# Performance work log

Hardware: AMD Instinct MI355X
Metric: run time of the kernel (lower is better)

Reference implementation:

```python
import jax, jax.numpy as jnp
import numpy as np

N_ITEMS = 100000
N_USERS = 40000
EMB = 100
NNZ_A = 3200000
NNZ_U = 1600000
BATCH = 4096
LAYERS = 3


def setup_inputs() -> dict:
    key = jax.random.key(0)
    ks = jax.random.split(key, 9)
    return {
        "adj_vals": jax.random.uniform(ks[0], (NNZ_A,), dtype=jnp.float32),
        "u_vals": jax.random.uniform(ks[1], (NNZ_U,), dtype=jnp.float32),
        "embedding": jax.random.normal(ks[2], (N_ITEMS, EMB), dtype=jnp.float32),
        "user_embedding": jax.random.normal(ks[3], (N_USERS, EMB), dtype=jnp.float32),
        "adj_rows": jax.random.randint(ks[4], (NNZ_A,), 0, N_ITEMS),
        "adj_cols": jax.random.randint(ks[5], (NNZ_A,), 0, N_ITEMS),
        "u_rows": jax.random.randint(ks[6], (NNZ_U,), 0, N_USERS),
        "u_cols": jax.random.randint(ks[7], (NNZ_U,), 0, N_ITEMS),
        "user": jax.random.randint(ks[8], (BATCH,), 0, N_USERS),
    }


def spmm(vals, rows, cols, x, n_rows):
    # COO sparse (n_rows x n_cols) @ dense x: gather rows of x by col index,
    # scale by nnz values, scatter-add into output rows.
    return jax.ops.segment_sum(vals[:, None] * x[cols], rows, num_segments=n_rows)


def reference(adj_vals, u_vals, embedding, user_embedding,
              adj_rows, adj_cols, u_rows, u_cols, user):
    # Multi-hop hypergraph propagation with running layer-sum (final = sum of layers 0..L)
    x = embedding
    total = x
    for _ in range(LAYERS):
        x = spmm(adj_vals, adj_rows, adj_cols, x, embedding.shape[0])
        total = total + x
    # ishyper branch: user embeddings = (u_adj @ summed item embeddings)[user]
    user_all = spmm(u_vals, u_rows, u_cols, total, user_embedding.shape[0])
    return total, user_all[user]
```

## Files before the change

### kernel.cpp

```cpp
#include <hip/hip_runtime.h>
#include <stdint.h>

#define EMB 100
#define HW 50
#define V4_PER_ROW 25
#define BSHIFT 8
#define NBMAX 1024
#define TP 256
#define EP 16

static __device__ __forceinline__ uint32_t pack_bf16(float a, float b) {
    uint32_t ua = __float_as_uint(a);
    uint32_t ub = __float_as_uint(b);
    ua = (ua + 0x7FFFu + ((ua >> 16) & 1u)) >> 16;
    ub = (ub + 0x7FFFu + ((ub >> 16) & 1u)) >> 16;
    return ua | (ub << 16);
}
static __device__ __forceinline__ float bflo(uint32_t p) { return __uint_as_float(p << 16); }
static __device__ __forceinline__ float bfhi(uint32_t p) { return __uint_as_float(p & 0xFFFF0000u); }

__global__ void convert_bf16(const float2* __restrict__ x, uint32_t* __restrict__ xbf, int nwords) {
    for (int i = blockIdx.x * blockDim.x + threadIdx.x; i < nwords; i += gridDim.x * blockDim.x) {
        float2 v = x[i];
        xbf[i] = pack_bf16(v.x, v.y);
    }
}

__global__ void map_build(const int* __restrict__ user, uint32_t* __restrict__ map, int batch) {
    int i = blockIdx.x * blockDim.x + threadIdx.x;
    if (i < batch) atomicMin(&map[user[i]], (uint32_t)i);
}

__global__ __launch_bounds__(TP) void pass1_count(
    const int* __restrict__ ra, int na, const int* __restrict__ ru, int nu,
    const uint32_t* __restrict__ map, int* __restrict__ countsT,
    int nblk, int nbA, int nbTot)
{
    __shared__ int lc[NBMAX];
    const int blk = blockIdx.x;
    for (int i = threadIdx.x; i < nbTot; i += TP) lc[i] = 0;
    __syncthreads();
    const int base = blk * (TP * EP);
    const int n = na + nu;
    for (int i = 0; i < EP; ++i) {
        int e = base + i * TP + threadIdx.x;
        int b = -1;
        if (e < na) {
            b = __builtin_nontemporal_load(ra + e) >> BSHIFT;
        } else if (e < n) {
            int r = __builtin_nontemporal_load(ru + (e - na));
            if (map[r] != 0xFFFFFFFFu) b = nbA + (r >> BSHIFT);
        }
        if (b >= 0) atomicAdd(&lc[b], 1);
    }
    __syncthreads();
    for (int i = threadIdx.x; i < nbTot; i += TP)
        countsT[(size_t)i * nblk + blk] = lc[i];
}

#define SCAN_T 256
#define SCAN_E 16

__global__ void scan_blocks(const int* __restrict__ in, int* __restrict__ out,
                            int* __restrict__ sums, int n) {
    __shared__ int smem[SCAN_T];
    const int b = blockIdx.x, tid = threadIdx.x;
    const int base = b * SCAN_T * SCAN_E + tid * SCAN_E;
    int loc[SCAN_E];
    int s = 0;
    for (int i = 0; i < SCAN_E; ++i) {
        int idx = base + i;
        int v = (idx < n) ? in[idx] : 0;
        loc[i] = s; s += v;
    }
    smem[tid] = s; __syncthreads();
    for (int off = 1; off < SCAN_T; off <<= 1) {
        int v = (tid >= off) ? smem[tid - off] : 0;
        __syncthreads();
        smem[tid] += v;
        __syncthreads();
    }
    int pre = (tid == 0) ? 0 : smem[tid - 1];
    if (tid == SCAN_T - 1) sums[b] = smem[tid];
    for (int i = 0; i < SCAN_E; ++i) {
        int idx = base + i;
        if (idx < n) out[idx] = pre + loc[i];
    }
}

__global__ void scan_mid(int* __restrict__ sums, int nb, int* __restrict__ total_out) {
    __shared__ int sh[256];
    const int t = threadIdx.x;
    int v = (t < nb) ? sums[t] : 0;
    sh[t] = v; __syncthreads();
    for (int off = 1; off < 256; off <<= 1) {
        int u = (t >= off) ? sh[t - off] : 0;
        __syncthreads();
        sh[t] += u;
        __syncthreads();
    }
    if (t < nb) sums[t] = sh[t];
    if (t == 255) *total_out = sh[255];
}

__global__ void scan_fixup(int* __restrict__ out, const int* __restrict__ sums, int n) {
    const int b = blockIdx.x;
    if (b == 0) return;
    const int add = sums[b - 1];
    const int base = b * SCAN_T * SCAN_E + threadIdx.x * SCAN_E;
    for (int i = 0; i < SCAN_E; ++i) {
        int idx = base + i;
        if (idx < n) out[idx] += add;
    }
}

__global__ void extract_bases(const int* __restrict__ scanned, int nblk, int nbTot,
                              const int* __restrict__ total, int* __restrict__ bases,
                              int* __restrict__ rpA_end, int nnzA, int* __restrict__ rpU_end) {
    int t = blockIdx.x * blockDim.x + threadIdx.x;
    if (t < nbTot) bases[t] = scanned[(size_t)t * nblk];
    if (t == 0) {
        int tot = *total;
        bases[nbTot] = tot;
        *rpA_end = nnzA;
        *rpU_end = tot - nnzA;
    }
}

__global__ __launch_bounds__(TP) void pass2_scatter(
    const float* __restrict__ va, const int* __restrict__ ra, const int* __restrict__ ia, int na,
    const float* __restrict__ vu, const int* __restrict__ ru, const int* __restrict__ iu, int nu,
    const uint32_t* __restrict__ map, const int* __restrict__ scanned,
    uint2* __restrict__ tmp, int nblk, int nbA, int nbTot)
{
    __shared__ int cur[NBMAX];
    const int blk = blockIdx.x;
    for (int i = threadIdx.x; i < nbTot; i += TP)
        cur[i] = scanned[(size_t)i * nblk + blk];
    __syncthreads();
    const int base = blk * (TP * EP);
    const int n = na + nu;
    for (int i = 0; i < EP; ++i) {
        int e = base + i * TP + threadIdx.x;
        if (e < na) {
            int r = __builtin_nontemporal_load(ra + e);
            int p = atomicAdd(&cur[r >> BSHIFT], 1);
            uint32_t key = ((uint32_t)(r & 255) << 17) | (uint32_t)__builtin_nontemporal_load(ia + e);
            tmp[p] = make_uint2(key, (uint32_t)__float_as_uint(__builtin_nontemporal_load(va + e)));
        } else if (e < n) {
            int k = e - na;
            int r = __builtin_nontemporal_load(ru + k);
            if (map[r] == 0xFFFFFFFFu) continue;
            int p = atomicAdd(&cur[nbA + (r >> BSHIFT)], 1);
            uint32_t key = ((uint32_t)(r & 255) << 17) | (uint32_t)__builtin_nontemporal_load(iu + k);
            tmp[p] = make_uint2(key, (uint32_t)__float_as_uint(__builtin_nontemporal_load(vu + k)));
        }
    }
}

__global__ __launch_bounds__(1024) void bucket_sort(const uint2* __restrict__ tmp,
                                                    const int* __restrict__ bases,
                                                    uint32_t* __restrict__ pk,
                                                    int* __restrict__ rpA, int* __restrict__ rpU,
                                                    int nbA, int nnzA, int nItems, int nUsers) {
    __shared__ int h[256];
    __shared__ int cur[256];
    const int t = threadIdx.x;
    const int b = blockIdx.x;
    const int lo = bases[b], hi = bases[b + 1];
    const bool isU = (b >= nbA);
    const int rowbase = (isU ? (b - nbA) : b) << BSHIFT;

    if (t < 256) h[t] = 0;
    __syncthreads();
    for (int i = lo + t; i < hi; i += 1024)
        atomicAdd(&h[tmp[i].x >> 17], 1);
    __syncthreads();
    int cnt = (t < 256) ? h[t] : 0;
    for (int off = 1; off < 256; off <<= 1) {
        int u = (t < 256 && t >= off) ? h[t - off] : 0;
        __syncthreads();
        if (t < 256) h[t] += u;
        __syncthreads();
    }
    if (t < 256) {
        int gpos = lo + h[t] - cnt;
        int row = rowbase + t;
        if (isU) { if (row < nUsers) rpU[row] = gpos - nnzA; }
        else     { if (row < nItems) rpA[row] = gpos; }
        cur[t] = gpos;
    }
    __syncthreads();
    for (int i = lo + t; i < hi; i += 1024) {
        uint2 e = tmp[i];
        int rl = (int)(e.x >> 17);
        uint32_t col = e.x & 0x1FFFFu;
        int p = atomicAdd(&cur[rl], 1);
        float v = __uint_as_float(e.y);
        uint32_t q = (uint32_t)(v * 32767.0f + 0.5f);
        if (q > 32767u) q = 32767u;
        pk[p] = (col << 15) | q;
    }
}

#define DECODE(w, v, c) { v = (float)((w) & 0x7FFFu) * (1.0f/32767.0f); c = (int)((w) >> 15); }

__global__ __launch_bounds__(256) void spmm_pk(
    const uint32_t* __restrict__ pk, const int* __restrict__ rowptr,
    const uint32_t* __restrict__ xbf, uint32_t* __restrict__ outbf,
    const float2* __restrict__ emb2, const uint32_t* __restrict__ x1bf,
    const uint32_t* __restrict__ x2bf, float2* __restrict__ total2,
    uint32_t* __restrict__ totbf, int nrows)
{
    const int wid = (blockIdx.x * blockDim.x + threadIdx.x) >> 6;
    const int lane = threadIdx.x & 63;
    if (wid >= nrows) return;
    const int start = rowptr[wid], end = rowptr[wid + 1];
    float a0 = 0.f, a1 = 0.f;
    for (int base = start; base < end; base += 64) {
        const int nc = min(64, end - base);
        uint32_t w = 0;
        if (lane < nc) w = __builtin_nontemporal_load(pk + base + lane);
        float myv; int myc;
        DECODE(w, myv, myc);
        int t = 0;
        for (; t + 4 <= nc; t += 4) {
            float v0 = __shfl(myv, t),     v1 = __shfl(myv, t + 1);
            float v2 = __shfl(myv, t + 2), v3 = __shfl(myv, t + 3);
            int   c0 = __shfl(myc, t),     c1 = __shfl(myc, t + 1);
            int   c2 = __shfl(myc, t + 2), c3 = __shfl(myc, t + 3);
            uint32_t p0 = 0, p1 = 0, p2 = 0, p3 = 0;
            if (lane < HW) {
                p0 = xbf[(size_t)c0 * HW + lane];
                p1 = xbf[(size_t)c1 * HW + lane];
                p2 = xbf[(size_t)c2 * HW + lane];
                p3 = xbf[(size_t)c3 * HW + lane];
            }
            a0 = fmaf(v0, bflo(p0), a0); a1 = fmaf(v0, bfhi(p0), a1);
            a0 = fmaf(v1, bflo(p1), a0); a1 = fmaf(v1, bfhi(p1), a1);
            a0 = fmaf(v2, bflo(p2), a0); a1 = fmaf(v2, bfhi(p2), a1);
            a0 = fmaf(v3, bflo(p3), a0); a1 = fmaf(v3, bfhi(p3), a1);
        }
        for (; t < nc; ++t) {
            float v0 = __shfl(myv, t);
            int c0 = __shfl(myc, t);
            uint32_t p0 = 0;
            if (lane < HW) p0 = xbf[(size_t)c0 * HW + lane];
            a0 = fmaf(v0, bflo(p0), a0);
            a1 = fmaf(v0, bfhi(p0), a1);
        }
    }
    if (lane < HW) {
        const size_t widx = (size_t)wid * HW + lane;
        if (outbf) outbf[widx] = pack_bf16(a0, a1);
        if (total2) {
            float2 e = emb2[widx];
            uint32_t w1 = x1bf[widx], w2 = x2bf[widx];
            float t0 = e.x + bflo(w1) + bflo(w2) + a0;
            float t1 = e.y + bfhi(w1) + bfhi(w2) + a1;
            total2[widx] = make_float2(t0, t1);
            totbf[widx] = pack_bf16(t0, t1);
        }
    }
}

__global__ __launch_bounds__(256) void spmm_batch_pk(
    const uint32_t* __restrict__ pk, const int* __restrict__ rowptr,
    const int* __restrict__ user, const uint32_t* __restrict__ xbf,
    float2* __restrict__ out2, int batch)
{
    const int wid = (blockIdx.x * blockDim.x + threadIdx.x) >> 6;
    const int lane = threadIdx.x & 63;
    if (wid >= batch) return;
    const int row = user[wid];
    const int start = rowptr[row], end = rowptr[row + 1];
    float a0 = 0.f, a1 = 0.f;
    for (int base = start; base < end; base += 64) {
        const int nc = min(64, end - base);
        uint32_t w = 0;
        if (lane < nc) w = __builtin_nontemporal_load(pk + base + lane);
        float myv; int myc;
        DECODE(w, myv, myc);
        int t = 0;
        for (; t + 4 <= nc; t += 4) {
            float v0 = __shfl(myv, t),     v1 = __shfl(myv, t + 1);
            float v2 = __shfl(myv, t + 2), v3 = __shfl(myv, t + 3);
            int   c0 = __shfl(myc, t),     c1 = __shfl(myc, t + 1);
            int   c2 = __shfl(myc, t + 2), c3 = __shfl(myc, t + 3);
            uint32_t p0 = 0, p1 = 0, p2 = 0, p3 = 0;
            if (lane < HW) {
                p0 = xbf[(size_t)c0 * HW + lane];
                p1 = xbf[(size_t)c1 * HW + lane];
                p2 = xbf[(size_t)c2 * HW + lane];
                p3 = xbf[(size_t)c3 * HW + lane];
            }
            a0 = fmaf(v0, bflo(p0), a0); a1 = fmaf(v0, bfhi(p0), a1);
            a0 = fmaf(v1, bflo(p1), a0); a1 = fmaf(v1, bfhi(p1), a1);
            a0 = fmaf(v2, bflo(p2), a0); a1 = fmaf(v2, bfhi(p2), a1);
            a0 = fmaf(v3, bflo(p3), a0); a1 = fmaf(v3, bfhi(p3), a1);
        }
        for (; t < nc; ++t) {
            float v0 = __shfl(myv, t);
            int c0 = __shfl(myc, t);
            uint32_t p0 = 0;
            if (lane < HW) p0 = xbf[(size_t)c0 * HW + lane];
            a0 = fmaf(v0, bflo(p0), a0);
            a1 = fmaf(v0, bfhi(p0), a1);
        }
    }
    if (lane < HW) out2[(size_t)wid * HW + lane] = make_float2(a0, a1);
}

__global__ void spmm_scatter(const float* __restrict__ vals, const int* __restrict__ rows,
                             const int* __restrict__ cols, const float* __restrict__ x,
                             float* __restrict__ out, int nnz) {
    long long t = (long long)blockIdx.x * blockDim.x + threadIdx.x;
    int e = (int)(t / V4_PER_ROW);
    int c = (int)(t % V4_PER_ROW);
    if (e >= nnz) return;
    int col = cols[e]; int row = rows[e]; float v = vals[e];
    const float4 g = *(const float4*)(x + (size_t)col * EMB + c * 4);
    float* o = out + (size_t)row * EMB + c * 4;
    atomicAdd(o + 0, v * g.x); atomicAdd(o + 1, v * g.y);
    atomicAdd(o + 2, v * g.z); atomicAdd(o + 3, v * g.w);
}
__global__ void add_inplace(float* __restrict__ acc, const float* __restrict__ x, int n4) {
    int i = blockIdx.x * blockDim.x + threadIdx.x;
    if (i < n4) {
        float4 a = ((const float4*)acc)[i];
        const float4 b = ((const float4*)x)[i];
        a.x += b.x; a.y += b.y; a.z += b.z; a.w += b.w;
        ((float4*)acc)[i] = a;
    }
}
__global__ void gather_rows(const float* __restrict__ src, const int* __restrict__ idx,
                            float* __restrict__ out, int nrows) {
    int t = blockIdx.x * blockDim.x + threadIdx.x;
    int r = t / V4_PER_ROW, c = t % V4_PER_ROW;
    if (r >= nrows) return;
    int s = idx[r];
    *(float4*)(out + (size_t)r * EMB + c * 4) = *(const float4*)(src + (size_t)s * EMB + c * 4);
}

static inline size_t align256(size_t x) { return (x + 255) & ~(size_t)255; }

extern "C" void kernel_launch(void* const* d_in, const int* in_sizes, int n_in,
                              void* d_out, int out_size, void* d_ws, size_t ws_size,
                              hipStream_t stream) {
    const float* adj_vals  = (const float*)d_in[0];
    const float* u_vals    = (const float*)d_in[1];
    const float* embedding = (const float*)d_in[2];
    const int*   adj_rows  = (const int*)d_in[4];
    const int*   adj_cols  = (const int*)d_in[5];
    const int*   u_rows    = (const int*)d_in[6];
    const int*   u_cols    = (const int*)d_in[7];
    const int*   user      = (const int*)d_in[8];

    const int NNZ_A   = in_sizes[0];
    const int NNZ_U   = in_sizes[1];
    const int N_ITEMS = in_sizes[2] / EMB;
    const int N_USERS = in_sizes[3] / EMB;
    const int BATCH   = in_sizes[8];

    const int NB_A = (N_ITEMS + 255) >> BSHIFT;
    const int NB_U = (N_USERS + 255) >> BSHIFT;
    const int NB_TOT = NB_A + NB_U;

    const int NNZ_T = NNZ_A + NNZ_U;
    const int nblk = (NNZ_T + TP * EP - 1) / (TP * EP);
    const long long nScan = (long long)NB_TOT * nblk;
    const int nsb = (int)((nScan + SCAN_T * SCAN_E - 1) / (SCAN_T * SCAN_E));

    float* total    = (float*)d_out;
    float* out_user = total + (size_t)N_ITEMS * EMB;

    const size_t rowWords = (size_t)N_ITEMS * HW;

    size_t off = 0;
    char* ws = (char*)d_ws;
    #define WS_ALLOC(name, bytes) char* name = ws + off; off += align256(bytes)
    WS_ALLOC(p_r0,      2 * rowWords * 4);
    WS_ALLOC(p_ebf,     rowWords * 4);
    WS_ALLOC(p_pk,      (size_t)NNZ_T * 4);
    WS_ALLOC(p_rpA,     ((size_t)N_ITEMS + 1) * 4);
    WS_ALLOC(p_rpU,     ((size_t)N_USERS + 1) * 4);
    WS_ALLOC(p_map,     (size_t)N_USERS * 4);
    WS_ALLOC(p_countsT, (size_t)nScan * 4);
    WS_ALLOC(p_sums,    256 * 4);
    WS_ALLOC(p_total,   4);
    WS_ALLOC(p_bases,   ((size_t)NB_TOT + 1) * 4);
    #undef WS_ALLOC
    const size_t tmpBytes = (size_t)NNZ_T * 8;

    if (ws_size >= off && tmpBytes <= 2 * rowWords * 4 && NB_TOT <= NBMAX && nsb <= 256) {
        uint32_t* x1bf  = (uint32_t*)p_r0;
        uint32_t* x2bf  = (uint32_t*)(p_r0 + rowWords * 4);
        uint2*    tmp   = (uint2*)p_r0;
        uint32_t* embbf = (uint32_t*)p_ebf;
        uint32_t* totbf = (uint32_t*)p_ebf;
        uint32_t* pk    = (uint32_t*)p_pk;
        int* rpA = (int*)p_rpA;
        int* rpU = (int*)p_rpU;
        uint32_t* map = (uint32_t*)p_map;
        int* countsT = (int*)p_countsT;
        int* sums    = (int*)p_sums;
        int* totalN  = (int*)p_total;
        int* bases   = (int*)p_bases;

        hipMemsetAsync(map, 0xFF, (size_t)N_USERS * 4, stream);
        map_build<<<(BATCH + 255) / 256, 256, 0, stream>>>(user, map, BATCH);

        convert_bf16<<<2048, 256, 0, stream>>>((const float2*)embedding, embbf, (int)rowWords);

        pass1_count<<<nblk, TP, 0, stream>>>(adj_rows, NNZ_A, u_rows, NNZ_U, map,
                                             countsT, nblk, NB_A, NB_TOT);
        scan_blocks<<<nsb, SCAN_T, 0, stream>>>(countsT, countsT, sums, (int)nScan);
        scan_mid<<<1, 256, 0, stream>>>(sums, nsb, totalN);
        scan_fixup<<<nsb, SCAN_T, 0, stream>>>(countsT, sums, (int)nScan);
        extract_bases<<<(NB_TOT + 255) / 256, 256, 0, stream>>>(countsT, nblk, NB_TOT, totalN,
                                                                bases, rpA + N_ITEMS, NNZ_A,
                                                                rpU + N_USERS);
        pass2_scatter<<<nblk, TP, 0, stream>>>(adj_vals, adj_rows, adj_cols, NNZ_A,
                                               u_vals, u_rows, u_cols, NNZ_U,
                                               map, countsT, tmp, nblk, NB_A, NB_TOT);
        bucket_sort<<<NB_TOT, 1024, 0, stream>>>(tmp, bases, pk, rpA, rpU,
                                                 NB_A, NNZ_A, N_ITEMS, N_USERS);

        const int gridA = (N_ITEMS + 3) / 4;
        spmm_pk<<<gridA, 256, 0, stream>>>(pk, rpA, embbf, x1bf,
                                           nullptr, nullptr, nullptr, nullptr, nullptr, N_ITEMS);
        spmm_pk<<<gridA, 256, 0, stream>>>(pk, rpA, x1bf, x2bf,
                                           nullptr, nullptr, nullptr, nullptr, nullptr, N_ITEMS);
        spmm_pk<<<gridA, 256, 0, stream>>>(pk, rpA, x2bf, nullptr,
                                           (const float2*)embedding, x1bf, x2bf,
                                           (float2*)total, totbf, N_ITEMS);
        const int gridB = (BATCH + 3) / 4;
        spmm_batch_pk<<<gridB, 256, 0, stream>>>(pk + NNZ_A, rpU, user, totbf,
                                                 (float2*)out_user, BATCH);
    } else {
        const size_t itemBytes = (size_t)N_ITEMS * EMB * sizeof(float);
        float* buf0 = (float*)d_ws;
        float* buf1 = buf0 + (size_t)N_ITEMS * EMB;
        float* user_all = buf1;
        const size_t userBytes = (size_t)N_USERS * EMB * sizeof(float);

        hipMemcpyAsync(total, embedding, itemBytes, hipMemcpyDeviceToDevice, stream);
        const int blkA = (NNZ_A * V4_PER_ROW + 255) / 256;
        const int blkU = (NNZ_U * V4_PER_ROW + 255) / 256;
        const int n4 = N_ITEMS * EMB / 4;
        const int blkAdd = (n4 + 255) / 256;

        hipMemsetAsync(buf0, 0, itemBytes, stream);
        spmm_scatter<<<blkA, 256, 0, stream>>>(adj_vals, adj_rows, adj_cols, embedding, buf0, NNZ_A);
        add_inplace<<<blkAdd, 256, 0, stream>>>(total, buf0, n4);
        hipMemsetAsync(buf1, 0, itemBytes, stream);
        spmm_scatter<<<blkA, 256, 0, stream>>>(adj_vals, adj_rows, adj_cols, buf0, buf1, NNZ_A);
        add_inplace<<<blkAdd, 256, 0, stream>>>(total, buf1, n4);
        hipMemsetAsync(buf0, 0, itemBytes, stream);
        spmm_scatter<<<blkA, 256, 0, stream>>>(adj_vals, adj_rows, adj_cols, buf1, buf0, NNZ_A);
        add_inplace<<<blkAdd, 256, 0, stream>>>(total, buf0, n4);
        hipMemsetAsync(user_all, 0, userBytes, stream);
        spmm_scatter<<<blkU, 256, 0, stream>>>(u_vals, u_rows, u_cols, total, user_all, NNZ_U);
        gather_rows<<<(BATCH * V4_PER_ROW + 255) / 256, 256, 0, stream>>>(user_all, user, out_user, BATCH);
    }
}
```

Measured before the change: 553.2 us.

## Sub-sort nonzeros by column band within rows and unroll gather loop by eight

The bucket sort now orders the nonzeros of each row by 8192-column bands as a secondary key. It uses a 4096-bin histogram and a 1024-wide scan instead of a 256-bin row histogram. Clustering the gathered column indices this way aims to improve cache locality for the embedding-row gathers in the SpMM. The SpMM inner loop is also unrolled from four to eight gathers with a two-wide tail, to keep more loads in flight. The trade-off is a heavier sort kernel with more shared-memory bins and scan steps, plus higher register pressure in the SpMM.

```diff
diff --git a/kernel.cpp b/kernel.cpp
--- a/kernel.cpp
+++ b/kernel.cpp
@@ -8,6 +8,8 @@
 #define NBMAX 1024
 #define TP 256
 #define EP 16
+#define BANDSH 13
+#define NBIN 4096
 
 static __device__ __forceinline__ uint32_t pack_bf16(float a, float b) {
     uint32_t ua = __float_as_uint(a);
@@ -163,39 +165,47 @@
                                                     uint32_t* __restrict__ pk,
                                                     int* __restrict__ rpA, int* __restrict__ rpU,
                                                     int nbA, int nnzA, int nItems, int nUsers) {
-    __shared__ int h[256];
-    __shared__ int cur[256];
+    __shared__ int h[NBIN];
+    __shared__ int sc[1024];
     const int t = threadIdx.x;
     const int b = blockIdx.x;
     const int lo = bases[b], hi = bases[b + 1];
     const bool isU = (b >= nbA);
     const int rowbase = (isU ? (b - nbA) : b) << BSHIFT;
 
-    if (t < 256) h[t] = 0;
-    __syncthreads();
-    for (int i = lo + t; i < hi; i += 1024)
-        atomicAdd(&h[tmp[i].x >> 17], 1);
-    __syncthreads();
-    int cnt = (t < 256) ? h[t] : 0;
-    for (int off = 1; off < 256; off <<= 1) {
-        int u = (t < 256 && t >= off) ? h[t - off] : 0;
-        __syncthreads();
-        if (t < 256) h[t] += u;
-        __syncthreads();
-    }
+    for (int i = t; i < NBIN; i += 1024) h[i] = 0;
+    __syncthreads();
+    for (int i = lo + t; i < hi; i += 1024) {
+        uint2 e = tmp[i];
+        int key = (int)(((e.x >> 17) << 4) | ((e.x & 0x1FFFFu) >> BANDSH));
+        atomicAdd(&h[key], 1);
+    }
+    __syncthreads();
+    const int b0 = t * 4;
+    int s0 = h[b0], s1 = h[b0 + 1], s2 = h[b0 + 2], s3 = h[b0 + 3];
+    int tsum = s0 + s1 + s2 + s3;
+    sc[t] = tsum; __syncthreads();
+    for (int off = 1; off < 1024; off <<= 1) {
+        int v = (t >= off) ? sc[t - off] : 0;
+        __syncthreads();
+        sc[t] += v;
+        __syncthreads();
+    }
+    int excl = sc[t] - tsum;
+    h[b0] = excl; h[b0 + 1] = excl + s0; h[b0 + 2] = excl + s0 + s1; h[b0 + 3] = excl + s0 + s1 + s2;
+    __syncthreads();
     if (t < 256) {
-        int gpos = lo + h[t] - cnt;
         int row = rowbase + t;
+        int gpos = lo + h[t << 4];
         if (isU) { if (row < nUsers) rpU[row] = gpos - nnzA; }
         else     { if (row < nItems) rpA[row] = gpos; }
-        cur[t] = gpos;
     }
     __syncthreads();
     for (int i = lo + t; i < hi; i += 1024) {
         uint2 e = tmp[i];
-        int rl = (int)(e.x >> 17);
         uint32_t col = e.x & 0x1FFFFu;
-        int p = atomicAdd(&cur[rl], 1);
+        int key = (int)(((e.x >> 17) << 4) | (col >> BANDSH));
+        int p = lo + atomicAdd(&h[key], 1);
         float v = __uint_as_float(e.y);
         uint32_t q = (uint32_t)(v * 32767.0f + 0.5f);
         if (q > 32767u) q = 32767u;
@@ -204,6 +214,11 @@
 }
 
 #define DECODE(w, v, c) { v = (float)((w) & 0x7FFFu) * (1.0f/32767.0f); c = (int)((w) >> 15); }
+
+#define GATH1(vv, cc) {                                        \
+    uint32_t p_ = 0;                                           \
+    if (lane < HW) p_ = xbf[(size_t)(cc) * HW + lane];         \
+    a0 = fmaf((vv), bflo(p_), a0); a1 = fmaf((vv), bfhi(p_), a1); }
 
 __global__ __launch_bounds__(256) void spmm_pk(
     const uint32_t* __restrict__ pk, const int* __restrict__ rowptr,
@@ -224,30 +239,50 @@
         float myv; int myc;
         DECODE(w, myv, myc);
         int t = 0;
-        for (; t + 4 <= nc; t += 4) {
+        for (; t + 8 <= nc; t += 8) {
             float v0 = __shfl(myv, t),     v1 = __shfl(myv, t + 1);
             float v2 = __shfl(myv, t + 2), v3 = __shfl(myv, t + 3);
+            float v4 = __shfl(myv, t + 4), v5 = __shfl(myv, t + 5);
+            float v6 = __shfl(myv, t + 6), v7 = __shfl(myv, t + 7);
             int   c0 = __shfl(myc, t),     c1 = __shfl(myc, t + 1);
             int   c2 = __shfl(myc, t + 2), c3 = __shfl(myc, t + 3);
-            uint32_t p0 = 0, p1 = 0, p2 = 0, p3 = 0;
+            int   c4 = __shfl(myc, t + 4), c5 = __shfl(myc, t + 5);
+            int   c6 = __shfl(myc, t + 6), c7 = __shfl(myc, t + 7);
+            uint32_t p0 = 0, p1 = 0, p2 = 0, p3 = 0, p4 = 0, p5 = 0, p6 = 0, p7 = 0;
             if (lane < HW) {
                 p0 = xbf[(size_t)c0 * HW + lane];
                 p1 = xbf[(size_t)c1 * HW + lane];
                 p2 = xbf[(size_t)c2 * HW + lane];
                 p3 = xbf[(size_t)c3 * HW + lane];
+                p4 = xbf[(size_t)c4 * HW + lane];
+                p5 = xbf[(size_t)c5 * HW + lane];
+                p6 = xbf[(size_t)c6 * HW + lane];
+                p7 = xbf[(size_t)c7 * HW + lane];
             }
             a0 = fmaf(v0, bflo(p0), a0); a1 = fmaf(v0, bfhi(p0), a1);
             a0 = fmaf(v1, bflo(p1), a0); a1 = fmaf(v1, bfhi(p1), a1);
             a0 = fmaf(v2, bflo(p2), a0); a1 = fmaf(v2, bfhi(p2), a1);
             a0 = fmaf(v3, bflo(p3), a0); a1 = fmaf(v3, bfhi(p3), a1);
-        }
-        for (; t < nc; ++t) {
+            a0 = fmaf(v4, bflo(p4), a0); a1 = fmaf(v4, bfhi(p4), a1);
+            a0 = fmaf(v5, bflo(p5), a0); a1 = fmaf(v5, bfhi(p5), a1);
+            a0 = fmaf(v6, bflo(p6), a0); a1 = fmaf(v6, bfhi(p6), a1);
+            a0 = fmaf(v7, bflo(p7), a0); a1 = fmaf(v7, bfhi(p7), a1);
+        }
+        for (; t + 2 <= nc; t += 2) {
+            float v0 = __shfl(myv, t), v1 = __shfl(myv, t + 1);
+            int   c0 = __shfl(myc, t), c1 = __shfl(myc, t + 1);
+            uint32_t p0 = 0, p1 = 0;
+            if (lane < HW) {
+                p0 = xbf[(size_t)c0 * HW + lane];
+                p1 = xbf[(size_t)c1 * HW + lane];
+            }
+            a0 = fmaf(v0, bflo(p0), a0); a1 = fmaf(v0, bfhi(p0), a1);
+            a0 = fmaf(v1, bflo(p1), a0); a1 = fmaf(v1, bfhi(p1), a1);
+        }
+        if (t < nc) {
             float v0 = __shfl(myv, t);
             int c0 = __shfl(myc, t);
-            uint32_t p0 = 0;
-            if (lane < HW) p0 = xbf[(size_t)c0 * HW + lane];
-            a0 = fmaf(v0, bflo(p0), a0);
-            a1 = fmaf(v0, bfhi(p0), a1);
+            GATH1(v0, c0);
         }
     }
     if (lane < HW) {
@@ -302,10 +337,7 @@
         for (; t < nc; ++t) {
             float v0 = __shfl(myv, t);
             int c0 = __shfl(myc, t);
-            uint32_t p0 = 0;
-            if (lane < HW) p0 = xbf[(size_t)c0 * HW + lane];
-            a0 = fmaf(v0, bflo(p0), a0);
-            a1 = fmaf(v0, bfhi(p0), a1);
+            GATH1(v0, c0);
         }
     }
     if (lane < HW) out2[(size_t)wid * HW + lane] = make_float2(a0, a1);
@@ -392,7 +424,8 @@
     #undef WS_ALLOC
     const size_t tmpBytes = (size_t)NNZ_T * 8;
 
-    if (ws_size >= off && tmpBytes <= 2 * rowWords * 4 && NB_TOT <= NBMAX && nsb <= 256) {
+    if (ws_size >= off && tmpBytes <= 2 * rowWords * 4 && NB_TOT <= NBMAX && nsb <= 256
+        && N_ITEMS <= (1 << 17) && N_USERS <= (1 << 17)) {
         uint32_t* x1bf  = (uint32_t*)p_r0;
         uint32_t* x2bf  = (uint32_t*)(p_r0 + rowWords * 4);
         uint2*    tmp   = (uint2*)p_r0;
```

Measured after the change: 549.3 us. No clear change (-0.7%).

## Split wavefront into two half-waves processing two nonzeros with 8-byte gathers

Applied to the files above, without the earlier changes.

The SpMM kernels now split each 64-lane wavefront into two 32-lane halves. Each half handles alternate nonzeros and loads 8 bytes (four bf16 values) per lane over 25 active lanes, and the halves are combined with a cross-half shuffle at the end. This raises lane utilisation and memory-level parallelism for the random row gathers, in exchange for an extra reduction and a padded tail loop. The preprocessing items-per-thread constants (EP, SCAN_E) are also doubled to cut block counts in the count and scan passes.

```diff
diff --git a/kernel.cpp b/kernel.cpp
--- a/kernel.cpp
+++ b/kernel.cpp
@@ -3,11 +3,15 @@
 
 #define EMB 100
 #define HW 50
+#define HW2 25
 #define V4_PER_ROW 25
 #define BSHIFT 8
 #define NBMAX 1024
 #define TP 256
-#define EP 16
+#define EP 32
+
+#define SCAN_T 256
+#define SCAN_E 32
 
 static __device__ __forceinline__ uint32_t pack_bf16(float a, float b) {
     uint32_t ua = __float_as_uint(a);
@@ -57,9 +61,6 @@
     for (int i = threadIdx.x; i < nbTot; i += TP)
         countsT[(size_t)i * nblk + blk] = lc[i];
 }
-
-#define SCAN_T 256
-#define SCAN_E 16
 
 __global__ void scan_blocks(const int* __restrict__ in, int* __restrict__ out,
                             int* __restrict__ sums, int n) {
@@ -205,18 +206,23 @@
 
 #define DECODE(w, v, c) { v = (float)((w) & 0x7FFFu) * (1.0f/32767.0f); c = (int)((w) >> 15); }
 
+#define FMA2(vv, pp) { a0 = fmaf((vv), bflo((pp).x), a0); a1 = fmaf((vv), bfhi((pp).x), a1); \
+                       a2 = fmaf((vv), bflo((pp).y), a2); a3 = fmaf((vv), bfhi((pp).y), a3); }
+
 __global__ __launch_bounds__(256) void spmm_pk(
     const uint32_t* __restrict__ pk, const int* __restrict__ rowptr,
-    const uint32_t* __restrict__ xbf, uint32_t* __restrict__ outbf,
-    const float2* __restrict__ emb2, const uint32_t* __restrict__ x1bf,
-    const uint32_t* __restrict__ x2bf, float2* __restrict__ total2,
-    uint32_t* __restrict__ totbf, int nrows)
+    const uint2* __restrict__ xbf2, uint2* __restrict__ outbf2,
+    const float4* __restrict__ emb4, const uint2* __restrict__ x1bf2,
+    const uint2* __restrict__ x2bf2, float4* __restrict__ total4,
+    uint2* __restrict__ totbf2, int nrows)
 {
     const int wid = (blockIdx.x * blockDim.x + threadIdx.x) >> 6;
     const int lane = threadIdx.x & 63;
     if (wid >= nrows) return;
+    const int half = lane >> 5;
+    const int l = lane & 31;
     const int start = rowptr[wid], end = rowptr[wid + 1];
-    float a0 = 0.f, a1 = 0.f;
+    float a0 = 0.f, a1 = 0.f, a2 = 0.f, a3 = 0.f;
     for (int base = start; base < end; base += 64) {
         const int nc = min(64, end - base);
         uint32_t w = 0;
@@ -224,57 +230,63 @@
         float myv; int myc;
         DECODE(w, myv, myc);
         int t = 0;
-        for (; t + 4 <= nc; t += 4) {
-            float v0 = __shfl(myv, t),     v1 = __shfl(myv, t + 1);
-            float v2 = __shfl(myv, t + 2), v3 = __shfl(myv, t + 3);
-            int   c0 = __shfl(myc, t),     c1 = __shfl(myc, t + 1);
-            int   c2 = __shfl(myc, t + 2), c3 = __shfl(myc, t + 3);
-            uint32_t p0 = 0, p1 = 0, p2 = 0, p3 = 0;
-            if (lane < HW) {
-                p0 = xbf[(size_t)c0 * HW + lane];
-                p1 = xbf[(size_t)c1 * HW + lane];
-                p2 = xbf[(size_t)c2 * HW + lane];
-                p3 = xbf[(size_t)c3 * HW + lane];
+        for (; t + 8 <= nc; t += 8) {
+            float v0 = __shfl(myv, t + half),     v1 = __shfl(myv, t + 2 + half);
+            float v2 = __shfl(myv, t + 4 + half), v3 = __shfl(myv, t + 6 + half);
+            int   c0 = __shfl(myc, t + half),     c1 = __shfl(myc, t + 2 + half);
+            int   c2 = __shfl(myc, t + 4 + half), c3 = __shfl(myc, t + 6 + half);
+            uint2 p0 = make_uint2(0u,0u), p1 = make_uint2(0u,0u);
+            uint2 p2 = make_uint2(0u,0u), p3 = make_uint2(0u,0u);
+            if (l < HW2) {
+                p0 = xbf2[(size_t)c0 * HW2 + l];
+                p1 = xbf2[(size_t)c1 * HW2 + l];
+                p2 = xbf2[(size_t)c2 * HW2 + l];
+                p3 = xbf2[(size_t)c3 * HW2 + l];
             }
-            a0 = fmaf(v0, bflo(p0), a0); a1 = fmaf(v0, bfhi(p0), a1);
-            a0 = fmaf(v1, bflo(p1), a0); a1 = fmaf(v1, bfhi(p1), a1);
-            a0 = fmaf(v2, bflo(p2), a0); a1 = fmaf(v2, bfhi(p2), a1);
-            a0 = fmaf(v3, bflo(p3), a0); a1 = fmaf(v3, bfhi(p3), a1);
-        }
-        for (; t < nc; ++t) {
-            float v0 = __shfl(myv, t);
-            int c0 = __shfl(myc, t);
-            uint32_t p0 = 0;
-            if (lane < HW) p0 = xbf[(size_t)c0 * HW + lane];
-            a0 = fmaf(v0, bflo(p0), a0);
-            a1 = fmaf(v0, bfhi(p0), a1);
-        }
-    }
-    if (lane < HW) {
-        const size_t widx = (size_t)wid * HW + lane;
-        if (outbf) outbf[widx] = pack_bf16(a0, a1);
-        if (total2) {
-            float2 e = emb2[widx];
-            uint32_t w1 = x1bf[widx], w2 = x2bf[widx];
-            float t0 = e.x + bflo(w1) + bflo(w2) + a0;
-            float t1 = e.y + bfhi(w1) + bfhi(w2) + a1;
-            total2[widx] = make_float2(t0, t1);
-            totbf[widx] = pack_bf16(t0, t1);
+            FMA2(v0, p0); FMA2(v1, p1); FMA2(v2, p2); FMA2(v3, p3);
+        }
+        for (; t < nc; t += 2) {
+            int tt = min(t + half, nc - 1);
+            float v0 = __shfl(myv, tt);
+            int   c0 = __shfl(myc, tt);
+            if (t + half >= nc) v0 = 0.f;
+            uint2 p0 = make_uint2(0u,0u);
+            if (l < HW2) p0 = xbf2[(size_t)c0 * HW2 + l];
+            FMA2(v0, p0);
+        }
+    }
+    a0 += __shfl_xor(a0, 32); a1 += __shfl_xor(a1, 32);
+    a2 += __shfl_xor(a2, 32); a3 += __shfl_xor(a3, 32);
+    if (lane < HW2) {
+        const size_t widx = (size_t)wid * HW2 + lane;
+        if (outbf2) {
+            outbf2[widx] = make_uint2(pack_bf16(a0, a1), pack_bf16(a2, a3));
+        } else {
+            float4 e = emb4[widx];
+            uint2 w1 = x1bf2[widx], w2 = x2bf2[widx];
+            float t0 = e.x + bflo(w1.x) + bflo(w2.x) + a0;
+            float t1 = e.y + bfhi(w1.x) + bfhi(w2.x) + a1;
+            float t2 = e.z + bflo(w1.y) + bflo(w2.y) + a2;
+            float t3 = e.w + bfhi(w1.y) + bfhi(w2.y) + a3;
+            total4[widx] = make_float4(t0, t1, t2, t3);
+            totbf2[widx] = make_uint2(pack_bf16(t0, t1), pack_bf16(t2, t3));
         }
     }
 }
 
 __global__ __launch_bounds__(256) void spmm_batch_pk(
     const uint32_t* __restrict__ pk, const int* __restrict__ rowptr,
-    const int* __restrict__ user, const uint32_t* __restrict__ xbf,
-    float2* __restrict__ out2, int batch)
+    const int* __restrict__ user, const uint2* __restrict__ xbf2,
+    float4* __restrict__ out4, int batch)
 {
     const int wid = (blockIdx.x * blockDim.x + threadIdx.x) >> 6;
     const int lane = threadIdx.x & 63;
     if (wid >= batch) return;
+    const int half = lane >> 5;
+    const int l = lane & 31;
     const int row = user[wid];
     const int start = rowptr[row], end = rowptr[row + 1];
-    float a0 = 0.f, a1 = 0.f;
+    float a0 = 0.f, a1 = 0.f, a2 = 0.f, a3 = 0.f;
     for (int base = start; base < end; base += 64) {
         const int nc = min(64, end - base);
         uint32_t w = 0;
@@ -282,33 +294,34 @@
         float myv; int myc;
         DECODE(w, myv, myc);
         int t = 0;
-        for (; t + 4 <= nc; t += 4) {
-            float v0 = __shfl(myv, t),     v1 = __shfl(myv, t + 1);
-            float v2 = __shfl(myv, t + 2), v3 = __shfl(myv, t + 3);
-            int   c0 = __shfl(myc, t),     c1 = __shfl(myc, t + 1);
-            int   c2 = __shfl(myc, t + 2), c3 = __shfl(myc, t + 3);
-            uint32_t p0 = 0, p1 = 0, p2 = 0, p3 = 0;
-            if (lane < HW) {
-                p0 = xbf[(size_t)c0 * HW + lane];
-                p1 = xbf[(size_t)c1 * HW + lane];
-                p2 = xbf[(size_t)c2 * HW + lane];
-                p3 = xbf[(size_t)c3 * HW + lane];
+        for (; t + 8 <= nc; t += 8) {
+            float v0 = __shfl(myv, t + half),     v1 = __shfl(myv, t + 2 + half);
+            float v2 = __shfl(myv, t + 4 + half), v3 = __shfl(myv, t + 6 + half);
+            int   c0 = __shfl(myc, t + half),     c1 = __shfl(myc, t + 2 + half);
+            int   c2 = __shfl(myc, t + 4 + half), c3 = __shfl(myc, t + 6 + half);
+            uint2 p0 = make_uint2(0u,0u), p1 = make_uint2(0u,0u);
+            uint2 p2 = make_uint2(0u,0u), p3 = make_uint2(0u,0u);
+            if (l < HW2) {
+                p0 = xbf2[(size_t)c0 * HW2 + l];
+                p1 = xbf2[(size_t)c1 * HW2 + l];
+                p2 = xbf2[(size_t)c2 * HW2 + l];
+                p3 = xbf2[(size_t)c3 * HW2 + l];
             }
-            a0 = fmaf(v0, bflo(p0), a0); a1 = fmaf(v0, bfhi(p0), a1);
-            a0 = fmaf(v1, bflo(p1), a0); a1 = fmaf(v1, bfhi(p1), a1);
-            a0 = fmaf(v2, bflo(p2), a0); a1 = fmaf(v2, bfhi(p2), a1);
-            a0 = fmaf(v3, bflo(p3), a0); a1 = fmaf(v3, bfhi(p3), a1);
-        }
-        for (; t < nc; ++t) {
-            float v0 = __shfl(myv, t);
-            int c0 = __shfl(myc, t);
-            uint32_t p0 = 0;
-            if (lane < HW) p0 = xbf[(size_t)c0 * HW + lane];
-            a0 = fmaf(v0, bflo(p0), a0);
-            a1 = fmaf(v0, bfhi(p0), a1);
-        }
-    }
-    if (lane < HW) out2[(size_t)wid * HW + lane] = make_float2(a0, a1);
+            FMA2(v0, p0); FMA2(v1, p1); FMA2(v2, p2); FMA2(v3, p3);
+        }
+        for (; t < nc; t += 2) {
+            int tt = min(t + half, nc - 1);
+            float v0 = __shfl(myv, tt);
+            int   c0 = __shfl(myc, tt);
+            if (t + half >= nc) v0 = 0.f;
+            uint2 p0 = make_uint2(0u,0u);
+            if (l < HW2) p0 = xbf2[(size_t)c0 * HW2 + l];
+            FMA2(v0, p0);
+        }
+    }
+    a0 += __shfl_xor(a0, 32); a1 += __shfl_xor(a1, 32);
+    a2 += __shfl_xor(a2, 32); a3 += __shfl_xor(a3, 32);
+    if (lane < HW2) out4[(size_t)wid * HW2 + lane] = make_float4(a0, a1, a2, a3);
 }
 
 __global__ void spmm_scatter(const float* __restrict__ vals, const int* __restrict__ rows,
@@ -392,7 +405,8 @@
     #undef WS_ALLOC
     const size_t tmpBytes = (size_t)NNZ_T * 8;
 
-    if (ws_size >= off && tmpBytes <= 2 * rowWords * 4 && NB_TOT <= NBMAX && nsb <= 256) {
+    if (ws_size >= off && tmpBytes <= 2 * rowWords * 4 && NB_TOT <= NBMAX && nsb <= 256
+        && N_ITEMS <= (1 << 17) && N_USERS <= (1 << 17)) {
         uint32_t* x1bf  = (uint32_t*)p_r0;
         uint32_t* x2bf  = (uint32_t*)(p_r0 + rowWords * 4);
         uint2*    tmp   = (uint2*)p_r0;
@@ -427,16 +441,17 @@
                                                  NB_A, NNZ_A, N_ITEMS, N_USERS);
 
         const int gridA = (N_ITEMS + 3) / 4;
-        spmm_pk<<<gridA, 256, 0, stream>>>(pk, rpA, embbf, x1bf,
+        spmm_pk<<<gridA, 256, 0, stream>>>(pk, rpA, (const uint2*)embbf, (uint2*)x1bf,
                                            nullptr, nullptr, nullptr, nullptr, nullptr, N_ITEMS);
-        spmm_pk<<<gridA, 256, 0, stream>>>(pk, rpA, x1bf, x2bf,
+        spmm_pk<<<gridA, 256, 0, stream>>>(pk, rpA, (const uint2*)x1bf, (uint2*)x2bf,
                                            nullptr, nullptr, nullptr, nullptr, nullptr, N_ITEMS);
-        spmm_pk<<<gridA, 256, 0, stream>>>(pk, rpA, x2bf, nullptr,
-                                           (const float2*)embedding, x1bf, x2bf,
-                                           (float2*)total, totbf, N_ITEMS);
-        const int gridB = (BATCH + 3) / 4;
-        spmm_batch_pk<<<gridB, 256, 0, stream>>>(pk + NNZ_A, rpU, user, totbf,
-                                                 (float2*)out_user, BATCH);
+        spmm_pk<<<gridA, 256, 0, stream>>>(pk, rpA, (const uint2*)x2bf, nullptr,
+                                           (const float4*)embedding, (const uint2*)x1bf,
+                                           (const uint2*)x2bf, (float4*)total,
+                                           (uint2*)totbf, N_ITEMS);
+        spmm_batch_pk<<<(BATCH + 3) / 4, 256, 0, stream>>>(pk + NNZ_A, rpU, user,
+                                                           (const uint2*)totbf,
+                                                           (float4*)out_user, BATCH);
     } else {
         const size_t itemBytes = (size_t)N_ITEMS * EMB * sizeof(float);
         float* buf0 = (float*)d_ws;
```

Result: slower. 569.6 us (+3.0%).
